# Kernel tuning notes

Hardware: AMD Instinct MI355X
Metric: run time of the kernel (lower is better)

Reference implementation:

```python
import jax, jax.numpy as jnp
import numpy as np

B, C, H, W = 4, 3, 1024, 1024
RADII = (8, 16, 32, 64)
EPS = 1e-5  # BatchNorm2d default eps


def _box_sum(x, r, s):
    # depthwise all-ones conv (kernel r, stride s, VALID padding) == summed box
    return jax.lax.reduce_window(x, 0.0, jax.lax.add, (1, 1, r, r), (1, 1, s, s), 'VALID')


def _axis_interp_ac(x, n_out, axis):
    # bilinear (align_corners=True) interpolation along one axis
    n_in = x.shape[axis]
    pos = jnp.arange(n_out, dtype=x.dtype) * ((n_in - 1) / max(n_out - 1, 1))
    i0 = jnp.clip(jnp.floor(pos).astype(jnp.int32), 0, n_in - 2)
    w = pos - i0.astype(x.dtype)
    a = jnp.take(x, i0, axis=axis)
    b = jnp.take(x, i0 + 1, axis=axis)
    shape = [1] * x.ndim
    shape[axis] = n_out
    w = w.reshape(shape)
    return a * (1 - w) + b * w


def _resize_ac(x, oh, ow):
    x = _axis_interp_ac(x, oh, 2)
    x = _axis_interp_ac(x, ow, 3)
    return x


def _bn(x, g, b, rm, rv):
    inv = g / jnp.sqrt(rv + EPS)
    return x * inv[None, :, None, None] + (b - rm * inv)[None, :, None, None]


def _forward(guide, src, w1, g1, b1, rm1, rv1, w2, g2, b2, rm2, rv2, w3):
    Hg, Wg = guide.shape[2], guide.shape[3]
    gg = guide * guide
    gs = guide * src
    ones = jnp.ones((1, guide.shape[1], Hg, Wg), guide.dtype)
    stats = []
    for r in RADII:
        s = r // 2
        N = _box_sum(ones, r, s)
        mx = _box_sum(guide, r, s) / N
        my = _box_sum(src, r, s) / N
        cov = _box_sum(gs, r, s) / N - mx * my
        var = _box_sum(gg, r, s) / N - mx * mx
        stats.append((mx, my, cov, var))
    mx1, my1, cov1, var1 = stats[0]
    oh, ow = cov1.shape[2], cov1.shape[3]
    feats = [cov1, var1]
    for (_, _, cov, var) in stats[1:]:
        feats.append(_resize_ac(cov, oh, ow))
        feats.append(_resize_ac(var, oh, ow))
    x = jnp.concatenate(feats, axis=1)  # [B,24,oh,ow]
    x = jax.nn.relu(_bn(jnp.einsum('oc,bchw->bohw', w1, x), g1, b1, rm1, rv1))
    x = jax.nn.relu(_bn(jnp.einsum('oc,bchw->bohw', w2, x), g2, b2, rm2, rv2))
    A = jnp.einsum('oc,bchw->bohw', w3, x)  # [B,3,oh,ow]
    bb = my1 - A * mx1
    mean_A = _resize_ac(A, Hg, Wg)
    mean_b = _resize_ac(bb, Hg, Wg)
    return mean_A * guide + mean_b


def setup_inputs() -> dict:
    key = jax.random.key(0)
    ks = jax.random.split(key, 5)
    f32 = jnp.float32
    return {
        'guide': jax.random.normal(ks[0], (B, C, H, W), f32),
        'src': jax.random.normal(ks[1], (B, C, H, W), f32),
        'w1': jax.random.normal(ks[2], (48, 24), f32) * 0.05,
        'g1': jnp.ones((48,), f32), 'b1': jnp.zeros((48,), f32),
        'rm1': jnp.zeros((48,), f32), 'rv1': jnp.ones((48,), f32),
        'w2': jax.random.normal(ks[3], (48, 48), f32) * 0.05,
        'g2': jnp.ones((48,), f32), 'b2': jnp.zeros((48,), f32),
        'rm2': jnp.zeros((48,), f32), 'rv2': jnp.ones((48,), f32),
        'w3': jax.random.normal(ks[4], (3, 48), f32) * 0.05,
    }


def reference(guide, src, w1, g1, b1, rm1, rv1, w2, g2, b2, rm2, rv2, w3):
    return _forward(guide, src, w1, g1, b1, rm1, rv1, w2, g2, b2, rm2, rv2, w3)
```

## Files before the change

### kernel.cpp

```cpp
#include <hip/hip_runtime.h>

#define HH 1024
#define WW 1024
#define NB 4
#define NC 3
#define BC 12
#define N1 255
#define N2 127
#define N3 63
#define N4 31
#define EPS 1e-5f

constexpr size_t S8_OFF  = 0;
constexpr size_t S8_SZ   = 4ull * BC * N1 * N1;
constexpr size_t S16_OFF = S8_OFF + S8_SZ;
constexpr size_t S16_SZ  = 4ull * BC * N2 * N2;
constexpr size_t S32_OFF = S16_OFF + S16_SZ;
constexpr size_t S32_SZ  = 4ull * BC * N3 * N3;
constexpr size_t S64_OFF = S32_OFF + S32_SZ;
constexpr size_t S64_SZ  = 4ull * BC * N4 * N4;
constexpr size_t CV16_OFF = S64_OFF + S64_SZ;
constexpr size_t CV16_SZ  = 2ull * BC * N2 * N2;
constexpr size_t CV32_OFF = CV16_OFF + CV16_SZ;
constexpr size_t CV32_SZ  = 2ull * BC * N3 * N3;
constexpr size_t CV64_OFF = CV32_OFF + CV32_SZ;
constexpr size_t CV64_SZ  = 2ull * BC * N4 * N4;
constexpr size_t A_OFF    = CV64_OFF + CV64_SZ;
constexpr size_t A_SZ     = (size_t)NB * NC * N1 * N1;
constexpr size_t BB_OFF   = A_OFF + A_SZ;
constexpr size_t WF_OFF   = BB_OFF + A_SZ;
constexpr int WF_W1 = 0;
constexpr int WF_B1 = 1152;
constexpr int WF_W2 = 1200;
constexpr int WF_B2 = 3504;
constexpr int WF_W3 = 3552;

__global__ __launch_bounds__(256) void prep_kernel(
    const float* __restrict__ w1, const float* __restrict__ g1,
    const float* __restrict__ b1, const float* __restrict__ rm1,
    const float* __restrict__ rv1,
    const float* __restrict__ w2, const float* __restrict__ g2,
    const float* __restrict__ b2, const float* __restrict__ rm2,
    const float* __restrict__ rv2,
    const float* __restrict__ w3, float* __restrict__ Wf)
{
    __shared__ float i1[48], i2[48];
    int t = threadIdx.x;
    if (t < 48) {
        float iv = g1[t] * rsqrtf(rv1[t] + EPS);
        i1[t] = iv;
        Wf[WF_B1 + t] = b1[t] - rm1[t] * iv;
        float iw = g2[t] * rsqrtf(rv2[t] + EPS);
        i2[t] = iw;
        Wf[WF_B2 + t] = b2[t] - rm2[t] * iw;
    }
    __syncthreads();
    for (int k = t; k < 48 * 24; k += 256) Wf[WF_W1 + k] = w1[k] * i1[k / 24];
    for (int k = t; k < 48 * 48; k += 256) Wf[WF_W2 + k] = w2[k] * i2[k / 48];
    for (int k = t; k < 3 * 48; k += 256)  Wf[WF_W3 + k] = w3[k];
}

__global__ __launch_bounds__(256) void base_kernel(
    const float* __restrict__ guide, const float* __restrict__ src,
    float* __restrict__ S8)
{
    int blk = blockIdx.x;
    int bc  = blk / 128;
    int i2  = blk % 128;
    int j   = threadIdx.x;
    if (j >= N1) return;

    int  row0 = 8 * i2;
    bool two  = (i2 < 127);

    const float* g0 = guide + (size_t)bc * HH * WW + (size_t)row0 * WW + 4 * j;
    const float* s0 = src   + (size_t)bc * HH * WW + (size_t)row0 * WW + 4 * j;

    float sg0 = 0.f, ss0 = 0.f, sgg0 = 0.f, sgs0 = 0.f;
    float sg1 = 0.f, ss1 = 0.f, sgg1 = 0.f, sgs1 = 0.f;

#pragma unroll
    for (int rr = 0; rr < 8; ++rr) {
        float4 ga = *(const float4*)(g0 + (size_t)rr * WW);
        float4 gb = *(const float4*)(g0 + (size_t)rr * WW + 4);
        float4 sa = *(const float4*)(s0 + (size_t)rr * WW);
        float4 sb = *(const float4*)(s0 + (size_t)rr * WW + 4);
        float ge[8] = {ga.x, ga.y, ga.z, ga.w, gb.x, gb.y, gb.z, gb.w};
        float se[8] = {sa.x, sa.y, sa.z, sa.w, sb.x, sb.y, sb.z, sb.w};
        float rg = 0.f, rs = 0.f, rgg = 0.f, rgs = 0.f;
#pragma unroll
        for (int k = 0; k < 8; ++k) {
            float g = ge[k], s = se[k];
            rg  += g;
            rs  += s;
            rgg += g * g;
            rgs += g * s;
        }
        sg0 += rg; ss0 += rs; sgg0 += rgg; sgs0 += rgs;
        if (rr >= 4) { sg1 += rg; ss1 += rs; sgg1 += rgg; sgs1 += rgs; }
    }
    if (two) {
#pragma unroll
        for (int rr = 8; rr < 12; ++rr) {
            float4 ga = *(const float4*)(g0 + (size_t)rr * WW);
            float4 gb = *(const float4*)(g0 + (size_t)rr * WW + 4);
            float4 sa = *(const float4*)(s0 + (size_t)rr * WW);
            float4 sb = *(const float4*)(s0 + (size_t)rr * WW + 4);
            float ge[8] = {ga.x, ga.y, ga.z, ga.w, gb.x, gb.y, gb.z, gb.w};
            float se[8] = {sa.x, sa.y, sa.z, sa.w, sb.x, sb.y, sb.z, sb.w};
            float rg = 0.f, rs = 0.f, rgg = 0.f, rgs = 0.f;
#pragma unroll
            for (int k = 0; k < 8; ++k) {
                float g = ge[k], s = se[k];
                rg  += g;
                rs  += s;
                rgg += g * g;
                rgs += g * s;
            }
            sg1 += rg; ss1 += rs; sgg1 += rgg; sgs1 += rgs;
        }
    }

    size_t qs   = (size_t)BC * N1 * N1;
    size_t idx0 = (size_t)bc * N1 * N1 + (size_t)(2 * i2) * N1 + j;
    S8[0 * qs + idx0] = sg0;
    S8[1 * qs + idx0] = ss0;
    S8[2 * qs + idx0] = sgg0;
    S8[3 * qs + idx0] = sgs0;
    if (two) {
        size_t idx1 = idx0 + N1;
        S8[0 * qs + idx1] = sg1;
        S8[1 * qs + idx1] = ss1;
        S8[2 * qs + idx1] = sgg1;
        S8[3 * qs + idx1] = sgs1;
    }
}

__global__ __launch_bounds__(256) void pyr_kernel(
    const float* __restrict__ Sin, float* __restrict__ Sout,
    float* __restrict__ CVout, int nin, int nout, float invN)
{
    int idx = blockIdx.x * blockDim.x + threadIdx.x;
    int total = BC * nout * nout;
    if (idx >= total) return;
    int j  = idx % nout;
    int t  = idx / nout;
    int i  = t % nout;
    int bc = t / nout;

    size_t sIn  = (size_t)BC * nin * nin;
    size_t base = (size_t)bc * nin * nin;
    int p = 2 * i, q = 2 * j;

    float sums[4];
#pragma unroll
    for (int qt = 0; qt < 4; ++qt) {
        const float* P = Sin + (size_t)qt * sIn + base;
        sums[qt] = P[(size_t)p * nin + q] + P[(size_t)(p + 2) * nin + q] +
                   P[(size_t)p * nin + q + 2] + P[(size_t)(p + 2) * nin + q + 2];
    }
    size_t sOut = (size_t)BC * nout * nout;
    size_t o    = (size_t)bc * nout * nout + (size_t)i * nout + j;
    Sout[0 * sOut + o] = sums[0];
    Sout[1 * sOut + o] = sums[1];
    Sout[2 * sOut + o] = sums[2];
    Sout[3 * sOut + o] = sums[3];
    float mx = sums[0] * invN, my = sums[1] * invN;
    CVout[o]        = sums[3] * invN - mx * my;
    CVout[sOut + o] = sums[2] * invN - mx * mx;
}

__global__ __launch_bounds__(256) void mlp_kernel(
    const float* __restrict__ S8,
    const float* __restrict__ CV16, const float* __restrict__ CV32,
    const float* __restrict__ CV64,
    const float* __restrict__ Wf,
    float* __restrict__ A, float* __restrict__ Bb)
{
    const float* __restrict__ W1 = Wf + WF_W1;
    const float* __restrict__ B1 = Wf + WF_B1;
    const float* __restrict__ W2 = Wf + WF_W2;
    const float* __restrict__ B2 = Wf + WF_B2;
    const float* __restrict__ W3 = Wf + WF_W3;

    int idx = blockIdx.x * 256 + threadIdx.x;
    if (idx >= NB * N1 * N1) return;
    int ox = idx % N1;
    int r  = idx / N1;
    int oy = r % N1;
    int b  = r / N1;

    float feats[24], mx1[3], my1[3];

    size_t s8q = (size_t)BC * N1 * N1;
    for (int c = 0; c < 3; ++c) {
        size_t o = (size_t)(b * 3 + c) * N1 * N1 + (size_t)oy * N1 + ox;
        float sg = S8[o], ss = S8[s8q + o], sgg = S8[2 * s8q + o], sgs = S8[3 * s8q + o];
        float mx = sg * (1.f / 64.f), my = ss * (1.f / 64.f);
        mx1[c] = mx; my1[c] = my;
        feats[c]     = sgs * (1.f / 64.f) - mx * my;
        feats[3 + c] = sgg * (1.f / 64.f) - mx * mx;
    }

    const float* CVs[3] = {CV16, CV32, CV64};
    const int nins[3]   = {N2, N3, N4};
    const float scales[3] = {(float)(126.0 / 254.0), (float)(62.0 / 254.0),
                             (float)(30.0 / 254.0)};
#pragma unroll
    for (int l = 0; l < 3; ++l) {
        const float* CV = CVs[l];
        int nin = nins[l];
        float sc = scales[l];
        float py = (float)oy * sc;
        int   i0 = min(max((int)floorf(py), 0), nin - 2);
        float wy = py - (float)i0;
        float px = (float)ox * sc;
        int   j0 = min(max((int)floorf(px), 0), nin - 2);
        float wx = px - (float)j0;
        size_t cvq = (size_t)BC * nin * nin;
        int fo = 6 + 6 * l;
        for (int c = 0; c < 3; ++c) {
            size_t bix = (size_t)(b * 3 + c) * nin * nin;
            size_t o00 = bix + (size_t)i0 * nin + j0;
            float c00 = CV[o00], c01 = CV[o00 + 1];
            float c10 = CV[o00 + nin], c11 = CV[o00 + nin + 1];
            feats[fo + c] = (c00 * (1.f - wy) + c10 * wy) * (1.f - wx) +
                            (c01 * (1.f - wy) + c11 * wy) * wx;
            float v00 = CV[cvq + o00], v01 = CV[cvq + o00 + 1];
            float v10 = CV[cvq + o00 + nin], v11 = CV[cvq + o00 + nin + 1];
            feats[fo + 3 + c] = (v00 * (1.f - wy) + v10 * wy) * (1.f - wx) +
                                (v01 * (1.f - wy) + v11 * wy) * wx;
        }
    }

    float h1[48];
#pragma unroll
    for (int o = 0; o < 48; ++o) {
        float acc = B1[o];
#pragma unroll
        for (int c = 0; c < 24; ++c) acc = fmaf(W1[o * 24 + c], feats[c], acc);
        h1[o] = fmaxf(acc, 0.f);
    }
    float h2[48];
#pragma unroll
    for (int o = 0; o < 48; ++o) {
        float acc = B2[o];
#pragma unroll
        for (int c = 0; c < 48; ++c) acc = fmaf(W2[o * 48 + c], h1[c], acc);
        h2[o] = fmaxf(acc, 0.f);
    }
#pragma unroll
    for (int c = 0; c < 3; ++c) {
        float acc = 0.f;
#pragma unroll
        for (int k = 0; k < 48; ++k) acc = fmaf(W3[c * 48 + k], h2[k], acc);
        size_t o = (size_t)(b * 3 + c) * N1 * N1 + (size_t)oy * N1 + ox;
        A[o]  = acc;
        Bb[o] = my1[c] - acc * mx1[c];
    }
}

__global__ __launch_bounds__(256) void final_kernel(
    const float* __restrict__ guide, const float* __restrict__ A,
    const float* __restrict__ Bb, float* __restrict__ out)
{
    __shared__ float aH[N1 + 1], bH[N1 + 1];
    int blk = blockIdx.x;
    int bc  = blk / HH;
    int h   = blk % HH;

    const float scale = (float)(254.0 / 1023.0);
    float py = (float)h * scale;
    int   i0 = min(max((int)floorf(py), 0), N1 - 2);
    float wy = py - (float)i0;

    int t = threadIdx.x;
    if (t < N1) {
        size_t base = (size_t)bc * N1 * N1 + (size_t)i0 * N1 + t;
        aH[t] = A[base] * (1.f - wy) + A[base + N1] * wy;
        bH[t] = Bb[base] * (1.f - wy) + Bb[base + N1] * wy;
    }
    __syncthreads();

    const float* gp = guide + (size_t)bc * HH * WW + (size_t)h * WW;
    float*       op = out   + (size_t)bc * HH * WW + (size_t)h * WW;

    float4 g4 = *(const float4*)(gp + 4 * t);
    float4 o4;
    float ge[4] = {g4.x, g4.y, g4.z, g4.w};
    float oe[4];
#pragma unroll
    for (int k = 0; k < 4; ++k) {
        int w = 4 * t + k;
        float px = (float)w * scale;
        int   j0 = min(max((int)floorf(px), 0), N1 - 2);
        float wx = px - (float)j0;
        float a = aH[j0] * (1.f - wx) + aH[j0 + 1] * wx;
        float bbv = bH[j0] * (1.f - wx) + bH[j0 + 1] * wx;
        oe[k] = a * ge[k] + bbv;
    }
    o4.x = oe[0]; o4.y = oe[1]; o4.z = oe[2]; o4.w = oe[3];
    *(float4*)(op + 4 * t) = o4;
}

extern "C" void kernel_launch(void* const* d_in, const int* in_sizes, int n_in,
                              void* d_out, int out_size, void* d_ws, size_t ws_size,
                              hipStream_t stream)
{
    const float* guide = (const float*)d_in[0];
    const float* src   = (const float*)d_in[1];
    const float* w1    = (const float*)d_in[2];
    const float* g1    = (const float*)d_in[3];
    const float* b1    = (const float*)d_in[4];
    const float* rm1   = (const float*)d_in[5];
    const float* rv1   = (const float*)d_in[6];
    const float* w2    = (const float*)d_in[7];
    const float* g2    = (const float*)d_in[8];
    const float* b2    = (const float*)d_in[9];
    const float* rm2   = (const float*)d_in[10];
    const float* rv2   = (const float*)d_in[11];
    const float* w3    = (const float*)d_in[12];
    float*       out   = (float*)d_out;

    float* ws   = (float*)d_ws;
    float* S8   = ws + S8_OFF;
    float* S16  = ws + S16_OFF;
    float* S32  = ws + S32_OFF;
    float* S64  = ws + S64_OFF;
    float* CV16 = ws + CV16_OFF;
    float* CV32 = ws + CV32_OFF;
    float* CV64 = ws + CV64_OFF;
    float* Abuf = ws + A_OFF;
    float* Bbuf = ws + BB_OFF;
    float* Wf   = ws + WF_OFF;

    prep_kernel<<<1, 256, 0, stream>>>(w1, g1, b1, rm1, rv1, w2, g2, b2, rm2, rv2,
                                       w3, Wf);

    base_kernel<<<BC * 128, 256, 0, stream>>>(guide, src, S8);

    {
        int total = BC * N2 * N2;
        pyr_kernel<<<(total + 255) / 256, 256, 0, stream>>>(S8, S16, CV16, N1, N2,
                                                            1.f / 256.f);
    }
    {
        int total = BC * N3 * N3;
        pyr_kernel<<<(total + 255) / 256, 256, 0, stream>>>(S16, S32, CV32, N2, N3,
                                                            1.f / 1024.f);
    }
    {
        int total = BC * N4 * N4;
        pyr_kernel<<<(total + 255) / 256, 256, 0, stream>>>(S32, S64, CV64, N3, N4,
                                                            1.f / 4096.f);
    }

    {
        int total = NB * N1 * N1;
        mlp_kernel<<<(total + 255) / 256, 256, 0, stream>>>(
            S8, CV16, CV32, CV64, Wf, Abuf, Bbuf);
    }

    final_kernel<<<BC * HH, 256, 0, stream>>>(guide, Abuf, Bbuf, out);
}
```

Baseline: 229.6 us.

## Split MLP output channels across two thread halves with shared-memory exchange

The per-pixel MLP is now computed by two threads per pixel. Each half of the block computes 24 of the 48 hidden channels per layer, the first-layer activations are exchanged through shared memory, and the partial third-layer sums are reduced there. This cuts per-thread register pressure (no 48-wide h1/h2 arrays) and the serial FMA chain length, which should improve occupancy and latency hiding. In exchange, feature gathering is duplicated across both halves and two block barriers plus shared-memory traffic are added.

```diff
diff --git a/kernel.cpp b/kernel.cpp
--- a/kernel.cpp
+++ b/kernel.cpp
@@ -183,80 +183,114 @@
     const float* __restrict__ B2 = Wf + WF_B2;
     const float* __restrict__ W3 = Wf + WF_W3;
 
-    int idx = blockIdx.x * 256 + threadIdx.x;
-    if (idx >= NB * N1 * N1) return;
-    int ox = idx % N1;
-    int r  = idx / N1;
-    int oy = r % N1;
-    int b  = r / N1;
+    __shared__ float H[128 * 51];
+
+    int t  = threadIdx.x;
+    int pl = t & 127;
+    int ob = 24 * __builtin_amdgcn_readfirstlane(t >> 7);
+
+    int  pixel = blockIdx.x * 128 + pl;
+    bool act   = pixel < NB * N1 * N1;
 
     float feats[24], mx1[3], my1[3];
-
-    size_t s8q = (size_t)BC * N1 * N1;
-    for (int c = 0; c < 3; ++c) {
-        size_t o = (size_t)(b * 3 + c) * N1 * N1 + (size_t)oy * N1 + ox;
-        float sg = S8[o], ss = S8[s8q + o], sgg = S8[2 * s8q + o], sgs = S8[3 * s8q + o];
-        float mx = sg * (1.f / 64.f), my = ss * (1.f / 64.f);
-        mx1[c] = mx; my1[c] = my;
-        feats[c]     = sgs * (1.f / 64.f) - mx * my;
-        feats[3 + c] = sgg * (1.f / 64.f) - mx * mx;
-    }
-
-    const float* CVs[3] = {CV16, CV32, CV64};
-    const int nins[3]   = {N2, N3, N4};
-    const float scales[3] = {(float)(126.0 / 254.0), (float)(62.0 / 254.0),
-                             (float)(30.0 / 254.0)};
-#pragma unroll
-    for (int l = 0; l < 3; ++l) {
-        const float* CV = CVs[l];
-        int nin = nins[l];
-        float sc = scales[l];
-        float py = (float)oy * sc;
-        int   i0 = min(max((int)floorf(py), 0), nin - 2);
-        float wy = py - (float)i0;
-        float px = (float)ox * sc;
-        int   j0 = min(max((int)floorf(px), 0), nin - 2);
-        float wx = px - (float)j0;
-        size_t cvq = (size_t)BC * nin * nin;
-        int fo = 6 + 6 * l;
+    size_t obase = 0;
+
+    if (act) {
+        int ox = pixel % N1;
+        int r  = pixel / N1;
+        int oy = r % N1;
+        int b  = r / N1;
+        obase = (size_t)(b * 3) * N1 * N1 + (size_t)oy * N1 + ox;
+
+        size_t s8q = (size_t)BC * N1 * N1;
+#pragma unroll
         for (int c = 0; c < 3; ++c) {
-            size_t bix = (size_t)(b * 3 + c) * nin * nin;
-            size_t o00 = bix + (size_t)i0 * nin + j0;
-            float c00 = CV[o00], c01 = CV[o00 + 1];
-            float c10 = CV[o00 + nin], c11 = CV[o00 + nin + 1];
-            feats[fo + c] = (c00 * (1.f - wy) + c10 * wy) * (1.f - wx) +
-                            (c01 * (1.f - wy) + c11 * wy) * wx;
-            float v00 = CV[cvq + o00], v01 = CV[cvq + o00 + 1];
-            float v10 = CV[cvq + o00 + nin], v11 = CV[cvq + o00 + nin + 1];
-            feats[fo + 3 + c] = (v00 * (1.f - wy) + v10 * wy) * (1.f - wx) +
-                                (v01 * (1.f - wy) + v11 * wy) * wx;
-        }
-    }
-
-    float h1[48];
-#pragma unroll
-    for (int o = 0; o < 48; ++o) {
-        float acc = B1[o];
-#pragma unroll
-        for (int c = 0; c < 24; ++c) acc = fmaf(W1[o * 24 + c], feats[c], acc);
-        h1[o] = fmaxf(acc, 0.f);
-    }
-    float h2[48];
-#pragma unroll
-    for (int o = 0; o < 48; ++o) {
-        float acc = B2[o];
-#pragma unroll
-        for (int c = 0; c < 48; ++c) acc = fmaf(W2[o * 48 + c], h1[c], acc);
-        h2[o] = fmaxf(acc, 0.f);
-    }
-#pragma unroll
-    for (int c = 0; c < 3; ++c) {
-        float acc = 0.f;
-#pragma unroll
-        for (int k = 0; k < 48; ++k) acc = fmaf(W3[c * 48 + k], h2[k], acc);
-        size_t o = (size_t)(b * 3 + c) * N1 * N1 + (size_t)oy * N1 + ox;
-        A[o]  = acc;
-        Bb[o] = my1[c] - acc * mx1[c];
+            size_t o = obase + (size_t)c * N1 * N1;
+            float sg = S8[o], ss = S8[s8q + o];
+            float sgg = S8[2 * s8q + o], sgs = S8[3 * s8q + o];
+            float mx = sg * (1.f / 64.f), my = ss * (1.f / 64.f);
+            mx1[c] = mx; my1[c] = my;
+            feats[c]     = sgs * (1.f / 64.f) - mx * my;
+            feats[3 + c] = sgg * (1.f / 64.f) - mx * mx;
+        }
+
+        const float* CVs[3] = {CV16, CV32, CV64};
+        const int nins[3]   = {N2, N3, N4};
+        const float scales[3] = {(float)(126.0 / 254.0), (float)(62.0 / 254.0),
+                                 (float)(30.0 / 254.0)};
+#pragma unroll
+        for (int l = 0; l < 3; ++l) {
+            const float* CV = CVs[l];
+            int nin = nins[l];
+            float sc = scales[l];
+            float py = (float)oy * sc;
+            int   i0 = min(max((int)floorf(py), 0), nin - 2);
+            float wy = py - (float)i0;
+            float px = (float)ox * sc;
+            int   j0 = min(max((int)floorf(px), 0), nin - 2);
+            float wx = px - (float)j0;
+            size_t cvq = (size_t)BC * nin * nin;
+            int fo = 6 + 6 * l;
+#pragma unroll
+            for (int c = 0; c < 3; ++c) {
+                size_t bix = (size_t)(b * 3 + c) * nin * nin;
+                size_t o00 = bix + (size_t)i0 * nin + j0;
+                float c00 = CV[o00], c01 = CV[o00 + 1];
+                float c10 = CV[o00 + nin], c11 = CV[o00 + nin + 1];
+                feats[fo + c] = (c00 * (1.f - wy) + c10 * wy) * (1.f - wx) +
+                                (c01 * (1.f - wy) + c11 * wy) * wx;
+                float v00 = CV[cvq + o00], v01 = CV[cvq + o00 + 1];
+                float v10 = CV[cvq + o00 + nin], v11 = CV[cvq + o00 + nin + 1];
+                feats[fo + 3 + c] = (v00 * (1.f - wy) + v10 * wy) * (1.f - wx) +
+                                    (v01 * (1.f - wy) + v11 * wy) * wx;
+            }
+        }
+
+#pragma unroll
+        for (int o = 0; o < 24; ++o) {
+            float acc = B1[ob + o];
+#pragma unroll
+            for (int c = 0; c < 24; ++c)
+                acc = fmaf(W1[(ob + o) * 24 + c], feats[c], acc);
+            H[pl * 51 + ob + o] = fmaxf(acc, 0.f);
+        }
+    }
+
+    __syncthreads();
+
+    float a3p[3] = {0.f, 0.f, 0.f};
+    if (act) {
+        float h1v[48];
+#pragma unroll
+        for (int c = 0; c < 48; ++c) h1v[c] = H[pl * 51 + c];
+
+#pragma unroll
+        for (int o = 0; o < 24; ++o) {
+            float acc = B2[ob + o];
+#pragma unroll
+            for (int c = 0; c < 48; ++c)
+                acc = fmaf(W2[(ob + o) * 48 + c], h1v[c], acc);
+            float h2 = fmaxf(acc, 0.f);
+#pragma unroll
+            for (int cc = 0; cc < 3; ++cc)
+                a3p[cc] = fmaf(W3[cc * 48 + ob + o], h2, a3p[cc]);
+        }
+        if (ob) {
+#pragma unroll
+            for (int cc = 0; cc < 3; ++cc) H[pl * 51 + 48 + cc] = a3p[cc];
+        }
+    }
+
+    __syncthreads();
+
+    if (act && ob == 0) {
+#pragma unroll
+        for (int cc = 0; cc < 3; ++cc) {
+            float a = a3p[cc] + H[pl * 51 + 48 + cc];
+            size_t o = obase + (size_t)cc * N1 * N1;
+            A[o]  = a;
+            Bb[o] = my1[cc] - a * mx1[cc];
+        }
     }
 }
 
@@ -356,8 +390,8 @@
     }
 
     {
-        int total = NB * N1 * N1;
-        mlp_kernel<<<(total + 255) / 256, 256, 0, stream>>>(
+        constexpr int TOTAL = NB * N1 * N1;
+        mlp_kernel<<<(TOTAL + 127) / 128, 256, 0, stream>>>(
             S8, CV16, CV32, CV64, Wf, Abuf, Bbuf);
     }
 
```

Result: slower. 236.7 us (+3.1%).
